# Kernel optimization log

Measured on AMD Instinct MI355X. Metric: run time of the kernel, lower is better.

Reference implementation:

```python
import jax, jax.numpy as jnp
import numpy as np

TEMPERATURE = 0.07


def setup_inputs() -> dict:
    key = jax.random.key(0)
    k1, k2, k3 = jax.random.split(key, 3)
    B, D = 8192, 256
    projections = jax.random.normal(k1, (B, D), dtype=jnp.float32)
    affordance_ids = jax.random.randint(k2, (B,), 0, 16, dtype=jnp.int64)
    instance_ids = jax.random.randint(k3, (B,), 0, 4096, dtype=jnp.int64)
    return {
        "projections": projections,
        "affordance_ids": affordance_ids,
        "instance_ids": instance_ids,
    }


def reference(projections, affordance_ids, instance_ids):
    B = projections.shape[0]
    # (B, B) similarity logits
    sim = jnp.matmul(projections, projections.T) / TEMPERATURE
    aff_mask = affordance_ids[:, None] == affordance_ids[None, :]
    inst_mask = instance_ids[:, None] == instance_ids[None, :]
    positive_mask = aff_mask & (~inst_mask)
    self_mask = jnp.eye(B, dtype=bool)
    # per-row logsumexp over all j != i (stable, single pass)
    masked_sim = jnp.where(self_mask, -jnp.inf, sim)
    lse = jax.nn.logsumexp(masked_sim, axis=1)  # (B,)
    # loss per positive pair: -sim[i,j] + lse[i]
    per_pair = jnp.where(positive_mask, lse[:, None] - sim, 0.0)
    num_pairs = jnp.sum(positive_mask)
    total = jnp.sum(per_pair)
    return jnp.where(num_pairs > 0, total / num_pairs.astype(sim.dtype), 0.0)
```

## Files before the change

kernel.cpp:

```cpp
#include <hip/hip_runtime.h>
#include <hip/hip_bf16.h>
#include <stdint.h>

#define BN 8192
#define DK 256
#define NCHUNK 4
#define JTILES 16
#define KLOG2E_T 20.609929155556617f
#define INV_T 14.285714285714286f
#define NEGINF (-3.0e38f)

typedef short vshort8 __attribute__((ext_vector_type(8)));
typedef float vfloat4 __attribute__((ext_vector_type(4)));

__device__ __forceinline__ void gload16(const void* g, void* lds) {
  __builtin_amdgcn_global_load_lds(
      (const __attribute__((address_space(1))) unsigned int*)g,
      (__attribute__((address_space(3))) unsigned int*)lds, 16, 0, 0);
}

__global__ __launch_bounds__(256) void prep_kernel(
    const float* __restrict__ P, const int* __restrict__ aff,
    const int* __restrict__ inst, ushort* __restrict__ Pb,
    int* __restrict__ keys) {
  int g = blockIdx.x * 256 + threadIdx.x;
  float4 f = ((const float4*)P)[g];
  ushort4 h;
  __hip_bfloat16 b;
  b = __float2bfloat16(f.x); h.x = __builtin_bit_cast(unsigned short, b);
  b = __float2bfloat16(f.y); h.y = __builtin_bit_cast(unsigned short, b);
  b = __float2bfloat16(f.z); h.z = __builtin_bit_cast(unsigned short, b);
  b = __float2bfloat16(f.w); h.w = __builtin_bit_cast(unsigned short, b);
  ((ushort4*)Pb)[g] = h;
  if (g < BN) keys[g] = (aff[g] << 12) | inst[g];
}

__global__ __launch_bounds__(512, 2) void fused_kernel(
    const ushort* __restrict__ Pb, const int* __restrict__ keys,
    float4* __restrict__ stats) {
  __shared__ __align__(16) ushort Abuf[4 * 128 * 64];
  __shared__ __align__(16) ushort Bbuf[2][128 * 64];
  __shared__ __align__(16) int jkeysL[2][128];

  const int tid = threadIdx.x;
  const int w = tid >> 6;
  const int l = tid & 63;
  const int q = l >> 4;
  const int li = l & 15;
  const int iw = w >> 1;
  const int jw = w & 1;

  const int bid = blockIdx.x;
  const int chunk = (bid & 7) >> 1;
  const int itile = ((bid >> 3) << 1) + (bid & 1);
  const int ibase = itile * 128;
  const int jcbase = chunk * 2048;

  const int gi0 = ibase + iw * 32 + li;
  const int gi1 = gi0 + 16;
  const int keyi0 = keys[gi0];
  const int keyi1 = keys[gi1];

  const ushort* gA = Pb + (size_t)ibase * DK;

  const int srow = tid >> 3;
  const size_t srcrow = (size_t)srow * (DK * 2);
  const int sboff = ((tid & 7) ^ (srow & 7)) * 16;
  const int wavebase = w << 10;

#pragma unroll
  for (int ks = 0; ks < 4; ++ks) {
#pragma unroll
    for (int qq = 0; qq < 2; ++qq) {
      gload16((const char*)gA + srcrow + (size_t)qq * 64 * (DK * 2) + ks * 128 + sboff,
              (char*)Abuf + ks * 16384 + qq * 8192 + wavebase);
    }
  }
  {
    const char* gB = (const char*)(Pb + (size_t)jcbase * DK);
    gload16(gB + srcrow + sboff, (char*)&Bbuf[0][0] + wavebase);
    gload16(gB + srcrow + (size_t)64 * (DK * 2) + sboff,
            (char*)&Bbuf[0][0] + 8192 + wavebase);
  }
  if (tid < 128) jkeysL[0][tid] = keys[jcbase + tid];
  __syncthreads();

  const int rowA0b = (iw * 32 + li) * 128;
  const int rowA1b = rowA0b + 2048;
  const int rowBb = (jw * 64 + li) * 128;
  const int swz0 = ((0 * 4 + q) ^ (l & 7)) * 16;
  const int swz1 = ((1 * 4 + q) ^ (l & 7)) * 16;

  float m0 = NEGINF, m1 = NEGINF, s0 = 0.f, s1 = 0.f;
  float ps0 = 0.f, ps1 = 0.f, pc0 = 0.f, pc1 = 0.f;

  for (int jt = 0; jt < JTILES; ++jt) {
    const int jtb = jcbase + jt * 128;
    vfloat4 acc[2][4];
#pragma unroll
    for (int a = 0; a < 2; ++a)
#pragma unroll
      for (int b = 0; b < 4; ++b) acc[a][b] = (vfloat4){0.f, 0.f, 0.f, 0.f};

#pragma unroll
    for (int ks = 0; ks < 4; ++ks) {
      if (ks < 3) {
        const char* gB = (const char*)(Pb + (size_t)jtb * DK);
        char* dst = (char*)&Bbuf[(ks + 1) & 1][0] + wavebase;
        gload16(gB + srcrow + (ks + 1) * 128 + sboff, dst);
        gload16(gB + srcrow + (size_t)64 * (DK * 2) + (ks + 1) * 128 + sboff, dst + 8192);
      }
      const char* As = (const char*)Abuf + ks * 16384;
      const char* Bs = (const char*)&Bbuf[ks & 1][0];
#pragma unroll
      for (int kk = 0; kk < 2; ++kk) {
        const int colo = kk ? swz1 : swz0;
        vshort8 i0 = *(const vshort8*)(As + rowA0b + colo);
        vshort8 i1 = *(const vshort8*)(As + rowA1b + colo);
#pragma unroll
        for (int fj = 0; fj < 4; ++fj) {
          vshort8 jv = *(const vshort8*)(Bs + rowBb + fj * 2048 + colo);
          acc[0][fj] = __builtin_amdgcn_mfma_f32_16x16x32_bf16(jv, i0, acc[0][fj], 0, 0, 0);
          acc[1][fj] = __builtin_amdgcn_mfma_f32_16x16x32_bf16(jv, i1, acc[1][fj], 0, 0, 0);
        }
      }
      __syncthreads();
    }

    if (jt + 1 < JTILES) {
      if (tid < 128) jkeysL[(jt + 1) & 1][tid] = keys[jtb + 128 + tid];
      const char* gB = (const char*)(Pb + (size_t)(jtb + 128) * DK);
      char* dst = (char*)&Bbuf[0][0] + wavebase;
      gload16(gB + srcrow + sboff, dst);
      gload16(gB + srcrow + (size_t)64 * (DK * 2) + sboff, dst + 8192);
    }

    const int iwb0 = ibase + iw * 32;
    float tmax0 = NEGINF, tmax1 = NEGINF;
#pragma unroll
    for (int fj = 0; fj < 4; ++fj) {
      const int jfb = jtb + jw * 64 + fj * 16;
      if (jfb == iwb0) {
#pragma unroll
        for (int r = 0; r < 4; ++r) {
          float v = acc[0][fj][r];
          v = (q * 4 + r == li) ? NEGINF : v;
          acc[0][fj][r] = v;
          tmax0 = fmaxf(tmax0, v);
        }
      } else {
#pragma unroll
        for (int r = 0; r < 4; ++r) tmax0 = fmaxf(tmax0, acc[0][fj][r]);
      }
      if (jfb == iwb0 + 16) {
#pragma unroll
        for (int r = 0; r < 4; ++r) {
          float v = acc[1][fj][r];
          v = (q * 4 + r == li) ? NEGINF : v;
          acc[1][fj][r] = v;
          tmax1 = fmaxf(tmax1, v);
        }
      } else {
#pragma unroll
        for (int r = 0; r < 4; ++r) tmax1 = fmaxf(tmax1, acc[1][fj][r]);
      }
    }
    tmax0 = fmaxf(tmax0, __shfl_xor(tmax0, 16));
    tmax0 = fmaxf(tmax0, __shfl_xor(tmax0, 32));
    tmax1 = fmaxf(tmax1, __shfl_xor(tmax1, 16));
    tmax1 = fmaxf(tmax1, __shfl_xor(tmax1, 32));
    const float mn0 = fmaxf(m0, tmax0);
    const float mn1 = fmaxf(m1, tmax1);
    s0 *= exp2f((m0 - mn0) * KLOG2E_T);
    s1 *= exp2f((m1 - mn1) * KLOG2E_T);
    m0 = mn0; m1 = mn1;
    const float rc0 = -mn0 * KLOG2E_T;
    const float rc1 = -mn1 * KLOG2E_T;
#pragma unroll
    for (int fj = 0; fj < 4; ++fj) {
      const int4 kj = *(const int4*)&jkeysL[jt & 1][jw * 64 + fj * 16 + q * 4];
      const int kja[4] = {kj.x, kj.y, kj.z, kj.w};
#pragma unroll
      for (int r = 0; r < 4; ++r) {
        const float v0 = acc[0][fj][r];
        const float v1 = acc[1][fj][r];
        s0 += exp2f(fmaf(v0, KLOG2E_T, rc0));
        s1 += exp2f(fmaf(v1, KLOG2E_T, rc1));
        const unsigned x0 = (unsigned)(kja[r] ^ keyi0);
        const unsigned x1 = (unsigned)(kja[r] ^ keyi1);
        const bool p0 = (x0 - 1u) < 4095u;
        const bool p1 = (x1 - 1u) < 4095u;
        ps0 += p0 ? v0 : 0.f;
        ps1 += p1 ? v1 : 0.f;
        pc0 += p0 ? 1.f : 0.f;
        pc1 += p1 ? 1.f : 0.f;
      }
    }
    __syncthreads();
  }

  s0 += __shfl_xor(s0, 16);  s0 += __shfl_xor(s0, 32);
  s1 += __shfl_xor(s1, 16);  s1 += __shfl_xor(s1, 32);
  ps0 += __shfl_xor(ps0, 16); ps0 += __shfl_xor(ps0, 32);
  ps1 += __shfl_xor(ps1, 16); ps1 += __shfl_xor(ps1, 32);
  pc0 += __shfl_xor(pc0, 16); pc0 += __shfl_xor(pc0, 32);
  pc1 += __shfl_xor(pc1, 16); pc1 += __shfl_xor(pc1, 32);
  if (l < 16) {
    const int slot = chunk * 2 + jw;
    stats[(size_t)slot * BN + gi0] = make_float4(m0, s0, ps0, pc0);
    stats[(size_t)slot * BN + gi1] = make_float4(m1, s1, ps1, pc1);
  }
}

__global__ __launch_bounds__(256) void reduce_rows(
    const float4* __restrict__ stats, float2* __restrict__ part) {
  const int i = blockIdx.x * 256 + threadIdx.x;
  float m = NEGINF, s = 0.f, ps = 0.f, pc = 0.f;
#pragma unroll
  for (int c = 0; c < 8; ++c) {
    float4 v = stats[(size_t)c * BN + i];
    float mn = fmaxf(m, v.x);
    s = s * exp2f((m - mn) * KLOG2E_T) + v.y * exp2f((v.x - mn) * KLOG2E_T);
    m = mn;
    ps += v.z;
    pc += v.w;
  }
  const float lse = m * INV_T + logf(s);
  float contrib = pc * lse - ps * INV_T;
#pragma unroll
  for (int off = 32; off > 0; off >>= 1) {
    contrib += __shfl_xor(contrib, off);
    pc += __shfl_xor(pc, off);
  }
  __shared__ float cs[4], pcs[4];
  if ((threadIdx.x & 63) == 0) {
    cs[threadIdx.x >> 6] = contrib;
    pcs[threadIdx.x >> 6] = pc;
  }
  __syncthreads();
  if (threadIdx.x == 0) {
    part[blockIdx.x] = make_float2(cs[0] + cs[1] + cs[2] + cs[3],
                                   pcs[0] + pcs[1] + pcs[2] + pcs[3]);
  }
}

__global__ void finalize(const float2* __restrict__ part, float* __restrict__ out) {
  float c = 0.f, p = 0.f;
  if (threadIdx.x < 32) {
    float2 v = part[threadIdx.x];
    c = v.x;
    p = v.y;
  }
#pragma unroll
  for (int off = 32; off > 0; off >>= 1) {
    c += __shfl_xor(c, off);
    p += __shfl_xor(p, off);
  }
  if (threadIdx.x == 0) out[0] = (p > 0.f) ? (c / p) : 0.f;
}

extern "C" void kernel_launch(void* const* d_in, const int* in_sizes, int n_in,
                              void* d_out, int out_size, void* d_ws, size_t ws_size,
                              hipStream_t stream) {
  const float* P = (const float*)d_in[0];
  const int* aff = (const int*)d_in[1];
  const int* inst = (const int*)d_in[2];
  char* ws = (char*)d_ws;
  ushort* Pb = (ushort*)ws;
  int* keys = (int*)(ws + 4 * 1024 * 1024);
  float4* stats = (float4*)(ws + 4 * 1024 * 1024 + 32768);
  float2* part = (float2*)(ws + 4 * 1024 * 1024 + 32768 + 8 * BN * 16);
  float* out = (float*)d_out;

  prep_kernel<<<2048, 256, 0, stream>>>(P, aff, inst, Pb, keys);
  fused_kernel<<<256, 512, 0, stream>>>(Pb, keys, stats);
  reduce_rows<<<32, 256, 0, stream>>>(stats, part);
  finalize<<<1, 64, 0, stream>>>(part, out);
}
```

Before: 75.40 us.

## Compute positive-pair sum algebraically via per-affordance sums and instance hash chains

The positive-pair similarity sum is no longer accumulated inside the GEMM loop. It is rewritten as p_i·G[aff] minus the same-instance terms, where G holds per-affordance column sums and the same-instance rows are walked through a hash-chain linked list built with atomics. This strips key loads and mask arithmetic from the fused logsumexp kernel, so i-tiles shrink to 64 rows, the grid doubles to 512 blocks with higher occupancy, and one barrier per tile is removed. In exchange it adds memsets, an accumulation kernel with float atomics, and a per-row pass over fp32 projections. The positive sums now use fp32 rather than bf16 similarities.

```diff
diff --git a/kernel.cpp b/kernel.cpp
--- a/kernel.cpp
+++ b/kernel.cpp
@@ -4,7 +4,6 @@
 
 #define BN 8192
 #define DK 256
-#define NCHUNK 4
 #define JTILES 16
 #define KLOG2E_T 20.609929155556617f
 #define INV_T 14.285714285714286f
@@ -22,7 +21,8 @@
 __global__ __launch_bounds__(256) void prep_kernel(
     const float* __restrict__ P, const int* __restrict__ aff,
     const int* __restrict__ inst, ushort* __restrict__ Pb,
-    int* __restrict__ keys) {
+    int* __restrict__ keys, int* __restrict__ head, int* __restrict__ nxt,
+    int* __restrict__ cntA) {
   int g = blockIdx.x * 256 + threadIdx.x;
   float4 f = ((const float4*)P)[g];
   ushort4 h;
@@ -32,15 +32,36 @@
   b = __float2bfloat16(f.z); h.z = __builtin_bit_cast(unsigned short, b);
   b = __float2bfloat16(f.w); h.w = __builtin_bit_cast(unsigned short, b);
   ((ushort4*)Pb)[g] = h;
-  if (g < BN) keys[g] = (aff[g] << 12) | inst[g];
-}
-
-__global__ __launch_bounds__(512, 2) void fused_kernel(
-    const ushort* __restrict__ Pb, const int* __restrict__ keys,
-    float4* __restrict__ stats) {
-  __shared__ __align__(16) ushort Abuf[4 * 128 * 64];
+  if (g < BN) {
+    int a = aff[g];
+    int k = (a << 12) | inst[g];
+    keys[g] = k;
+    nxt[g] = atomicExch(&head[k], g);
+    atomicAdd(&cntA[a], 1);
+  }
+}
+
+__global__ __launch_bounds__(256) void accum_g(
+    const float* __restrict__ P, const int* __restrict__ aff,
+    float* __restrict__ G) {
+  __shared__ float Gl[16 * 256];
+  const int t = threadIdx.x;
+#pragma unroll
+  for (int a = 0; a < 16; ++a) Gl[a * 256 + t] = 0.f;
+  const int r0 = blockIdx.x * 256;
+  for (int r = r0; r < r0 + 256; ++r) {
+    float v = P[(size_t)r * 256 + t];
+    int a = aff[r];
+    Gl[a * 256 + t] += v;
+  }
+#pragma unroll
+  for (int a = 0; a < 16; ++a) atomicAdd(&G[a * 256 + t], Gl[a * 256 + t]);
+}
+
+__global__ __launch_bounds__(512, 4) void fused_kernel(
+    const ushort* __restrict__ Pb, float2* __restrict__ stats) {
+  __shared__ __align__(16) ushort Abuf[4 * 64 * 64];
   __shared__ __align__(16) ushort Bbuf[2][128 * 64];
-  __shared__ __align__(16) int jkeysL[2][128];
 
   const int tid = threadIdx.x;
   const int w = tid >> 6;
@@ -53,210 +74,181 @@
   const int bid = blockIdx.x;
   const int chunk = (bid & 7) >> 1;
   const int itile = ((bid >> 3) << 1) + (bid & 1);
-  const int ibase = itile * 128;
+  const int ibase = itile * 64;
   const int jcbase = chunk * 2048;
 
-  const int gi0 = ibase + iw * 32 + li;
-  const int gi1 = gi0 + 16;
-  const int keyi0 = keys[gi0];
-  const int keyi1 = keys[gi1];
-
-  const ushort* gA = Pb + (size_t)ibase * DK;
+  const int gi = ibase + iw * 16 + li;
 
   const int srow = tid >> 3;
   const size_t srcrow = (size_t)srow * (DK * 2);
   const int sboff = ((tid & 7) ^ (srow & 7)) * 16;
-  const int wavebase = w << 10;
-
-#pragma unroll
-  for (int ks = 0; ks < 4; ++ks) {
-#pragma unroll
-    for (int qq = 0; qq < 2; ++qq) {
-      gload16((const char*)gA + srcrow + (size_t)qq * 64 * (DK * 2) + ks * 128 + sboff,
-              (char*)Abuf + ks * 16384 + qq * 8192 + wavebase);
-    }
-  }
+  const int dst16 = tid * 16;
+
+  const char* gA = (const char*)(Pb + (size_t)ibase * DK);
+#pragma unroll
+  for (int ks = 0; ks < 4; ++ks)
+    gload16(gA + srcrow + ks * 128 + sboff, (char*)Abuf + ks * 8192 + dst16);
   {
     const char* gB = (const char*)(Pb + (size_t)jcbase * DK);
-    gload16(gB + srcrow + sboff, (char*)&Bbuf[0][0] + wavebase);
+    gload16(gB + srcrow + sboff, (char*)&Bbuf[0][0] + dst16);
     gload16(gB + srcrow + (size_t)64 * (DK * 2) + sboff,
-            (char*)&Bbuf[0][0] + 8192 + wavebase);
-  }
-  if (tid < 128) jkeysL[0][tid] = keys[jcbase + tid];
+            (char*)&Bbuf[0][0] + 8192 + dst16);
+  }
   __syncthreads();
 
-  const int rowA0b = (iw * 32 + li) * 128;
-  const int rowA1b = rowA0b + 2048;
+  const int rowAb = (iw * 16 + li) * 128;
   const int rowBb = (jw * 64 + li) * 128;
-  const int swz0 = ((0 * 4 + q) ^ (l & 7)) * 16;
-  const int swz1 = ((1 * 4 + q) ^ (l & 7)) * 16;
-
-  float m0 = NEGINF, m1 = NEGINF, s0 = 0.f, s1 = 0.f;
-  float ps0 = 0.f, ps1 = 0.f, pc0 = 0.f, pc1 = 0.f;
+  const int swz0 = ((0 * 4 + q) ^ (li & 7)) * 16;
+  const int swz1 = ((1 * 4 + q) ^ (li & 7)) * 16;
+  const int iwb = ibase + iw * 16;
+
+  float m = NEGINF, sA = 0.f, sB = 0.f;
 
   for (int jt = 0; jt < JTILES; ++jt) {
     const int jtb = jcbase + jt * 128;
-    vfloat4 acc[2][4];
-#pragma unroll
-    for (int a = 0; a < 2; ++a)
-#pragma unroll
-      for (int b = 0; b < 4; ++b) acc[a][b] = (vfloat4){0.f, 0.f, 0.f, 0.f};
+    const char* gBj = (const char*)(Pb + (size_t)jtb * DK);
+    vfloat4 acc[4];
+#pragma unroll
+    for (int fj = 0; fj < 4; ++fj) acc[fj] = (vfloat4){0.f, 0.f, 0.f, 0.f};
 
 #pragma unroll
     for (int ks = 0; ks < 4; ++ks) {
       if (ks < 3) {
-        const char* gB = (const char*)(Pb + (size_t)jtb * DK);
-        char* dst = (char*)&Bbuf[(ks + 1) & 1][0] + wavebase;
-        gload16(gB + srcrow + (ks + 1) * 128 + sboff, dst);
-        gload16(gB + srcrow + (size_t)64 * (DK * 2) + (ks + 1) * 128 + sboff, dst + 8192);
+        char* dst = (char*)&Bbuf[(ks + 1) & 1][0] + dst16;
+        gload16(gBj + srcrow + (ks + 1) * 128 + sboff, dst);
+        gload16(gBj + srcrow + (size_t)64 * (DK * 2) + (ks + 1) * 128 + sboff,
+                dst + 8192);
       }
-      const char* As = (const char*)Abuf + ks * 16384;
+      const char* As = (const char*)Abuf + ks * 8192;
       const char* Bs = (const char*)&Bbuf[ks & 1][0];
 #pragma unroll
       for (int kk = 0; kk < 2; ++kk) {
         const int colo = kk ? swz1 : swz0;
-        vshort8 i0 = *(const vshort8*)(As + rowA0b + colo);
-        vshort8 i1 = *(const vshort8*)(As + rowA1b + colo);
+        vshort8 i0 = *(const vshort8*)(As + rowAb + colo);
 #pragma unroll
         for (int fj = 0; fj < 4; ++fj) {
           vshort8 jv = *(const vshort8*)(Bs + rowBb + fj * 2048 + colo);
-          acc[0][fj] = __builtin_amdgcn_mfma_f32_16x16x32_bf16(jv, i0, acc[0][fj], 0, 0, 0);
-          acc[1][fj] = __builtin_amdgcn_mfma_f32_16x16x32_bf16(jv, i1, acc[1][fj], 0, 0, 0);
+          acc[fj] = __builtin_amdgcn_mfma_f32_16x16x32_bf16(jv, i0, acc[fj], 0, 0, 0);
         }
       }
-      __syncthreads();
+      if (ks < 3) __syncthreads();
     }
 
     if (jt + 1 < JTILES) {
-      if (tid < 128) jkeysL[(jt + 1) & 1][tid] = keys[jtb + 128 + tid];
-      const char* gB = (const char*)(Pb + (size_t)(jtb + 128) * DK);
-      char* dst = (char*)&Bbuf[0][0] + wavebase;
+      const char* gB = gBj + 128 * (DK * 2);
+      char* dst = (char*)&Bbuf[0][0] + dst16;
       gload16(gB + srcrow + sboff, dst);
       gload16(gB + srcrow + (size_t)64 * (DK * 2) + sboff, dst + 8192);
     }
 
-    const int iwb0 = ibase + iw * 32;
-    float tmax0 = NEGINF, tmax1 = NEGINF;
+    float tmax = NEGINF;
 #pragma unroll
     for (int fj = 0; fj < 4; ++fj) {
-      const int jfb = jtb + jw * 64 + fj * 16;
-      if (jfb == iwb0) {
-#pragma unroll
-        for (int r = 0; r < 4; ++r) {
-          float v = acc[0][fj][r];
-          v = (q * 4 + r == li) ? NEGINF : v;
-          acc[0][fj][r] = v;
-          tmax0 = fmaxf(tmax0, v);
-        }
-      } else {
-#pragma unroll
-        for (int r = 0; r < 4; ++r) tmax0 = fmaxf(tmax0, acc[0][fj][r]);
+      const bool dia = (jtb + jw * 64 + fj * 16) == iwb;
+#pragma unroll
+      for (int r = 0; r < 4; ++r) {
+        float v = acc[fj][r];
+        if (dia && (q * 4 + r) == li) v = NEGINF;
+        acc[fj][r] = v;
+        tmax = fmaxf(tmax, v);
       }
-      if (jfb == iwb0 + 16) {
-#pragma unroll
-        for (int r = 0; r < 4; ++r) {
-          float v = acc[1][fj][r];
-          v = (q * 4 + r == li) ? NEGINF : v;
-          acc[1][fj][r] = v;
-          tmax1 = fmaxf(tmax1, v);
-        }
-      } else {
-#pragma unroll
-        for (int r = 0; r < 4; ++r) tmax1 = fmaxf(tmax1, acc[1][fj][r]);
-      }
-    }
-    tmax0 = fmaxf(tmax0, __shfl_xor(tmax0, 16));
-    tmax0 = fmaxf(tmax0, __shfl_xor(tmax0, 32));
-    tmax1 = fmaxf(tmax1, __shfl_xor(tmax1, 16));
-    tmax1 = fmaxf(tmax1, __shfl_xor(tmax1, 32));
-    const float mn0 = fmaxf(m0, tmax0);
-    const float mn1 = fmaxf(m1, tmax1);
-    s0 *= exp2f((m0 - mn0) * KLOG2E_T);
-    s1 *= exp2f((m1 - mn1) * KLOG2E_T);
-    m0 = mn0; m1 = mn1;
-    const float rc0 = -mn0 * KLOG2E_T;
-    const float rc1 = -mn1 * KLOG2E_T;
+    }
+    tmax = fmaxf(tmax, __shfl_xor(tmax, 16));
+    tmax = fmaxf(tmax, __shfl_xor(tmax, 32));
+    const float mn = fmaxf(m, tmax);
+    const float rs = exp2f((m - mn) * KLOG2E_T);
+    sA *= rs;
+    sB *= rs;
+    m = mn;
+    const float rc = -mn * KLOG2E_T;
 #pragma unroll
     for (int fj = 0; fj < 4; ++fj) {
-      const int4 kj = *(const int4*)&jkeysL[jt & 1][jw * 64 + fj * 16 + q * 4];
-      const int kja[4] = {kj.x, kj.y, kj.z, kj.w};
-#pragma unroll
-      for (int r = 0; r < 4; ++r) {
-        const float v0 = acc[0][fj][r];
-        const float v1 = acc[1][fj][r];
-        s0 += exp2f(fmaf(v0, KLOG2E_T, rc0));
-        s1 += exp2f(fmaf(v1, KLOG2E_T, rc1));
-        const unsigned x0 = (unsigned)(kja[r] ^ keyi0);
-        const unsigned x1 = (unsigned)(kja[r] ^ keyi1);
-        const bool p0 = (x0 - 1u) < 4095u;
-        const bool p1 = (x1 - 1u) < 4095u;
-        ps0 += p0 ? v0 : 0.f;
-        ps1 += p1 ? v1 : 0.f;
-        pc0 += p0 ? 1.f : 0.f;
-        pc1 += p1 ? 1.f : 0.f;
-      }
+      sA += exp2f(fmaf(acc[fj][0], KLOG2E_T, rc));
+      sB += exp2f(fmaf(acc[fj][1], KLOG2E_T, rc));
+      sA += exp2f(fmaf(acc[fj][2], KLOG2E_T, rc));
+      sB += exp2f(fmaf(acc[fj][3], KLOG2E_T, rc));
     }
     __syncthreads();
   }
 
-  s0 += __shfl_xor(s0, 16);  s0 += __shfl_xor(s0, 32);
-  s1 += __shfl_xor(s1, 16);  s1 += __shfl_xor(s1, 32);
-  ps0 += __shfl_xor(ps0, 16); ps0 += __shfl_xor(ps0, 32);
-  ps1 += __shfl_xor(ps1, 16); ps1 += __shfl_xor(ps1, 32);
-  pc0 += __shfl_xor(pc0, 16); pc0 += __shfl_xor(pc0, 32);
-  pc1 += __shfl_xor(pc1, 16); pc1 += __shfl_xor(pc1, 32);
+  float s = sA + sB;
+  s += __shfl_xor(s, 16);
+  s += __shfl_xor(s, 32);
   if (l < 16) {
     const int slot = chunk * 2 + jw;
-    stats[(size_t)slot * BN + gi0] = make_float4(m0, s0, ps0, pc0);
-    stats[(size_t)slot * BN + gi1] = make_float4(m1, s1, ps1, pc1);
-  }
-}
-
-__global__ __launch_bounds__(256) void reduce_rows(
-    const float4* __restrict__ stats, float2* __restrict__ part) {
-  const int i = blockIdx.x * 256 + threadIdx.x;
-  float m = NEGINF, s = 0.f, ps = 0.f, pc = 0.f;
-#pragma unroll
-  for (int c = 0; c < 8; ++c) {
-    float4 v = stats[(size_t)c * BN + i];
-    float mn = fmaxf(m, v.x);
-    s = s * exp2f((m - mn) * KLOG2E_T) + v.y * exp2f((v.x - mn) * KLOG2E_T);
-    m = mn;
-    ps += v.z;
-    pc += v.w;
-  }
-  const float lse = m * INV_T + logf(s);
-  float contrib = pc * lse - ps * INV_T;
-#pragma unroll
-  for (int off = 32; off > 0; off >>= 1) {
-    contrib += __shfl_xor(contrib, off);
-    pc += __shfl_xor(pc, off);
-  }
-  __shared__ float cs[4], pcs[4];
-  if ((threadIdx.x & 63) == 0) {
-    cs[threadIdx.x >> 6] = contrib;
-    pcs[threadIdx.x >> 6] = pc;
-  }
+    stats[(size_t)slot * BN + gi] = make_float2(m, s);
+  }
+}
+
+__global__ __launch_bounds__(256) void final_rows(
+    const float2* __restrict__ stats, const float* __restrict__ P,
+    const float* __restrict__ G, const int* __restrict__ keys,
+    const int* __restrict__ head, const int* __restrict__ nxt,
+    const int* __restrict__ cntA, float2* __restrict__ part) {
+  const int t = threadIdx.x;
+  const int rloc = t >> 6;
+  const int lane = t & 63;
+  const int i = blockIdx.x * 4 + rloc;
+
+  float2 st = stats[(size_t)(lane & 7) * BN + i];
+  float mm = st.x, ss = st.y;
+#pragma unroll
+  for (int off = 1; off < 8; off <<= 1) {
+    float mo = __shfl_xor(mm, off);
+    float so = __shfl_xor(ss, off);
+    float M = fmaxf(mm, mo);
+    ss = ss * exp2f((mm - M) * KLOG2E_T) + so * exp2f((mo - M) * KLOG2E_T);
+    mm = M;
+  }
+  const float lse = logf(ss) + mm * INV_T;
+
+  const int key = keys[i];
+  const int a = key >> 12;
+  float4 p4 = ((const float4*)(P + (size_t)i * 256))[lane];
+  float4 g4 = ((const float4*)(G + a * 256))[lane];
+  float acc = p4.x * g4.x + p4.y * g4.y + p4.z * g4.z + p4.w * g4.w;
+  int cnt = 0;
+  int j = head[key];
+  while (j >= 0) {
+    float4 q4 = ((const float4*)(P + (size_t)j * 256))[lane];
+    acc -= p4.x * q4.x + p4.y * q4.y + p4.z * q4.z + p4.w * q4.w;
+    cnt++;
+    j = nxt[j];
+  }
+#pragma unroll
+  for (int off = 1; off < 64; off <<= 1) acc += __shfl_xor(acc, off);
+  const float pc = (float)(cntA[a] - cnt);
+  const float contrib = pc * lse - acc * INV_T;
+
+  __shared__ float cs[4], ps[4];
+  if (lane == 0) { cs[rloc] = contrib; ps[rloc] = pc; }
   __syncthreads();
-  if (threadIdx.x == 0) {
+  if (t == 0)
     part[blockIdx.x] = make_float2(cs[0] + cs[1] + cs[2] + cs[3],
-                                   pcs[0] + pcs[1] + pcs[2] + pcs[3]);
-  }
+                                   ps[0] + ps[1] + ps[2] + ps[3]);
 }
 
 __global__ void finalize(const float2* __restrict__ part, float* __restrict__ out) {
+  const int t = threadIdx.x;
   float c = 0.f, p = 0.f;
-  if (threadIdx.x < 32) {
-    float2 v = part[threadIdx.x];
-    c = v.x;
-    p = v.y;
-  }
-#pragma unroll
-  for (int off = 32; off > 0; off >>= 1) {
+  for (int k = t; k < 2048; k += 256) {
+    float2 v = part[k];
+    c += v.x;
+    p += v.y;
+  }
+#pragma unroll
+  for (int off = 1; off < 64; off <<= 1) {
     c += __shfl_xor(c, off);
     p += __shfl_xor(p, off);
   }
-  if (threadIdx.x == 0) out[0] = (p > 0.f) ? (c / p) : 0.f;
+  __shared__ float cs[4], ps[4];
+  if ((t & 63) == 0) { cs[t >> 6] = c; ps[t >> 6] = p; }
+  __syncthreads();
+  if (t == 0) {
+    c = cs[0] + cs[1] + cs[2] + cs[3];
+    p = ps[0] + ps[1] + ps[2] + ps[3];
+    out[0] = (p > 0.f) ? (c / p) : 0.f;
+  }
 }
 
 extern "C" void kernel_launch(void* const* d_in, const int* in_sizes, int n_in,
@@ -266,14 +258,21 @@
   const int* aff = (const int*)d_in[1];
   const int* inst = (const int*)d_in[2];
   char* ws = (char*)d_ws;
-  ushort* Pb = (ushort*)ws;
-  int* keys = (int*)(ws + 4 * 1024 * 1024);
-  float4* stats = (float4*)(ws + 4 * 1024 * 1024 + 32768);
-  float2* part = (float2*)(ws + 4 * 1024 * 1024 + 32768 + 8 * BN * 16);
+  ushort* Pb   = (ushort*)(ws);
+  int*    keys = (int*)(ws + 4194304);
+  int*    head = (int*)(ws + 4227072);
+  int*    nxt  = (int*)(ws + 4489216);
+  float*  G    = (float*)(ws + 4521984);
+  int*    cntA = (int*)(ws + 4538368);
+  float2* stats = (float2*)(ws + 4538432);
+  float2* part = (float2*)(ws + 5062720);
   float* out = (float*)d_out;
 
-  prep_kernel<<<2048, 256, 0, stream>>>(P, aff, inst, Pb, keys);
-  fused_kernel<<<256, 512, 0, stream>>>(Pb, keys, stats);
-  reduce_rows<<<32, 256, 0, stream>>>(stats, part);
-  finalize<<<1, 64, 0, stream>>>(part, out);
-}
+  hipMemsetAsync(head, 0xFF, 65536 * 4, stream);
+  hipMemsetAsync(G, 0, 4096 * 4 + 64, stream);
+  prep_kernel<<<2048, 256, 0, stream>>>(P, aff, inst, Pb, keys, head, nxt, cntA);
+  accum_g<<<32, 256, 0, stream>>>(P, aff, G);
+  fused_kernel<<<512, 512, 0, stream>>>(Pb, stats);
+  final_rows<<<2048, 256, 0, stream>>>(stats, P, G, keys, head, nxt, cntA, part);
+  finalize<<<1, 256, 0, stream>>>(part, out);
+}
```

Result: slower. 111.9 us (+48.4%).
